# Optimization experiments

Measured on AMD Instinct MI355X. Metric: run time of the kernel, lower is better.

The kernel has to match this reference:

```python
import jax, jax.numpy as jnp
import numpy as np

N, E = 10000, 160000
IN_C, HID, OUT_C, H = 768, 256, 256, 4
EPS = 1e-5


def _gat_layer(x, src, dst, W, a_src, a_dst, b, n_nodes):
    # x: [N, Fin], W: [Fin, H*C], a_src/a_dst: [H, C], b: [C]
    h, c = a_src.shape
    xh = (x @ W).reshape(n_nodes, h, c)                      # [N,H,C]
    s = jnp.einsum('nhc,hc->nh', xh, a_src)                  # [N,H]
    d = jnp.einsum('nhc,hc->nh', xh, a_dst)                  # [N,H]
    e = jax.nn.leaky_relu(s[src] + d[dst], negative_slope=0.2)  # [E,H]
    # segment softmax over incoming edges of each dst node
    emax = jax.ops.segment_max(e, dst, num_segments=n_nodes)
    ex = jnp.exp(e - emax[dst])
    denom = jax.ops.segment_sum(ex, dst, num_segments=n_nodes)
    alpha = ex / denom[dst]                                  # [E,H]
    msg = alpha[:, :, None] * xh[src]                        # [E,H,C]
    out = jax.ops.segment_sum(msg, dst, num_segments=n_nodes)  # [N,H,C]
    return out.mean(axis=1) + b                              # concat=False: head mean


def setup_inputs() -> dict:
    key = jax.random.key(0)
    ks = jax.random.split(key, 12)
    sc1 = 1.0 / np.sqrt(IN_C)
    sc2 = 1.0 / np.sqrt(HID)
    return {
        'x': jax.random.normal(ks[0], (N, IN_C), dtype=jnp.float32),
        'edge_index': jax.random.randint(ks[1], (2, E), 0, N, dtype=jnp.int64),
        'W1': jax.random.normal(ks[2], (IN_C, H * HID), dtype=jnp.float32) * sc1,
        'att_src1': jax.random.normal(ks[3], (H, HID), dtype=jnp.float32) * sc2,
        'att_dst1': jax.random.normal(ks[4], (H, HID), dtype=jnp.float32) * sc2,
        'b1': jnp.zeros((HID,), dtype=jnp.float32),
        'gamma': jnp.ones((HID,), dtype=jnp.float32),
        'beta': jnp.zeros((HID,), dtype=jnp.float32),
        'W2': jax.random.normal(ks[5], (HID, H * OUT_C), dtype=jnp.float32) * sc2,
        'att_src2': jax.random.normal(ks[6], (H, OUT_C), dtype=jnp.float32) * sc2,
        'att_dst2': jax.random.normal(ks[7], (H, OUT_C), dtype=jnp.float32) * sc2,
        'b2': jnp.zeros((OUT_C,), dtype=jnp.float32),
    }


def reference(x, edge_index, W1, att_src1, att_dst1, b1, gamma, beta,
              W2, att_src2, att_dst2, b2):
    n = x.shape[0]
    loops = jnp.arange(n, dtype=edge_index.dtype)  # PyG GATConv adds self-loops
    src = jnp.concatenate([edge_index[0], loops])
    dst = jnp.concatenate([edge_index[1], loops])
    h = _gat_layer(x, src, dst, W1, att_src1, att_dst1, b1, n)   # [N,HID]
    # BatchNorm1d (batch statistics) + ReLU; dropout p=0 is identity
    mu = h.mean(axis=0)
    var = h.var(axis=0)
    h = (h - mu) * jax.lax.rsqrt(var + EPS) * gamma + beta
    h = jax.nn.relu(h)
    return _gat_layer(h, src, dst, W2, att_src2, att_dst2, b2, n)  # [N,OUT_C]
```

## Files before the change

### kernel.cpp

```cpp
#include <hip/hip_runtime.h>
#include <hip/hip_bf16.h>

typedef __bf16 bf16x8 __attribute__((ext_vector_type(8)));
typedef float f32x4 __attribute__((ext_vector_type(4)));
typedef unsigned short ushort8v __attribute__((ext_vector_type(8)));
typedef unsigned short ushort4v __attribute__((ext_vector_type(4)));

#define DEV __device__ __forceinline__

DEV unsigned short f2bf(float f) {
    unsigned u = __builtin_bit_cast(unsigned, f);
    unsigned r = (u + 0x7fffu + ((u >> 16) & 1u)) >> 16;
    return (unsigned short)r;
}

DEV float bf2f(unsigned short b) {
    unsigned u = ((unsigned)b) << 16;
    return __builtin_bit_cast(float, u);
}

DEV float wred_sum(float v) {
    #pragma unroll
    for (int o = 32; o > 0; o >>= 1) v += __shfl_xor(v, o, 64);
    return v;
}

__global__ __launch_bounds__(256) void cvtpad_k(const float* __restrict__ X,
                                                unsigned short* __restrict__ O,
                                                int nrows, int chunks, int ncols, int total) {
    int id = blockIdx.x * 256 + threadIdx.x;
    if (id >= total) return;
    int row = id / chunks;
    int k0 = (id - row * chunks) * 8;
    ushort8v o;
    if (row < nrows) {
        const float* p = X + (size_t)row * ncols + k0;
        float4 a = *(const float4*)p;
        float4 b = *(const float4*)(p + 4);
        o[0] = f2bf(a.x); o[1] = f2bf(a.y); o[2] = f2bf(a.z); o[3] = f2bf(a.w);
        o[4] = f2bf(b.x); o[5] = f2bf(b.y); o[6] = f2bf(b.z); o[7] = f2bf(b.w);
    } else {
        o = (ushort8v)0;
    }
    *(ushort8v*)(O + (size_t)id * 8) = o;
}

__global__ __launch_bounds__(256) void tr_k(const float* __restrict__ W,
                                            unsigned short* __restrict__ WT, int K, int F) {
    __shared__ unsigned short tile[32][33];
    int kb = blockIdx.x * 32, fb = blockIdx.y * 32;
    int tid = threadIdx.x;
    int c = tid & 31;
    #pragma unroll
    for (int i = 0; i < 4; i++) {
        int r = (tid >> 5) + i * 8;
        tile[r][c] = f2bf(W[(size_t)(kb + r) * F + fb + c]);
    }
    __syncthreads();
    #pragma unroll
    for (int i = 0; i < 4; i++) {
        int r = (tid >> 5) + i * 8;
        WT[(size_t)(fb + r) * K + kb + c] = tile[c][r];
    }
}

__global__ __launch_bounds__(256) void hist_k(const int* __restrict__ ei, int* __restrict__ count,
                                              int E, int Et) {
    int id = blockIdx.x * 256 + threadIdx.x;
    if (id >= Et) return;
    int dst = (id < E) ? ei[E + id] : (id - E);
    atomicAdd(&count[dst], 1);
}

__global__ __launch_bounds__(1024) void scan_k(const int* __restrict__ cnt, int* __restrict__ indptr,
                                               int* __restrict__ cursor, int n) {
    __shared__ int wsum[16];
    __shared__ int carry_s;
    int tid = threadIdx.x, wave = tid >> 6, lane = tid & 63;
    if (tid == 0) carry_s = 0;
    __syncthreads();
    for (int base = 0; base < n; base += 1024) {
        int v = (base + tid < n) ? cnt[base + tid] : 0;
        int s = v;
        #pragma unroll
        for (int o = 1; o < 64; o <<= 1) { int t = __shfl_up(s, o, 64); if (lane >= o) s += t; }
        if (lane == 63) wsum[wave] = s;
        __syncthreads();
        if (wave == 0 && lane < 16) {
            int ws = wsum[lane];
            #pragma unroll
            for (int o = 1; o < 16; o <<= 1) { int t = __shfl_up(ws, o, 64); if (lane >= o) ws += t; }
            wsum[lane] = ws;
        }
        __syncthreads();
        int excl = s - v + (wave > 0 ? wsum[wave - 1] : 0) + carry_s;
        if (base + tid < n) { indptr[base + tid] = excl; cursor[base + tid] = excl; }
        __syncthreads();
        if (tid == 0) carry_s += wsum[15];
        __syncthreads();
    }
    if (threadIdx.x == 0) indptr[n] = carry_s;
}

__global__ __launch_bounds__(256) void scatter_k(const int* __restrict__ ei, int* __restrict__ cursor,
                                                 int* __restrict__ srcs, int E, int Et) {
    int id = blockIdx.x * 256 + threadIdx.x;
    if (id >= Et) return;
    int s, d;
    if (id < E) { s = ei[id]; d = ei[E + id]; } else { s = id - E; d = s; }
    int pos = atomicAdd(&cursor[d], 1);
    srcs[pos] = s;
}

__global__ __launch_bounds__(256) void gemm_k(const unsigned short* __restrict__ A,
                                              const unsigned short* __restrict__ B,
                                              unsigned short* __restrict__ C, int K) {
    __shared__ unsigned short lds_a[128 * 64];
    __shared__ unsigned short lds_b[128 * 64];
    int m0 = blockIdx.x * 128, n0 = blockIdx.y * 128;
    int tid = threadIdx.x, wave = tid >> 6, lane = tid & 63;
    int wr = wave >> 1, wc = wave & 1;
    f32x4 acc[4][4] = {};
    int slotbase = wave * 256;
    for (int kt = 0; kt < K; kt += 64) {
        #pragma unroll
        for (int t = 0; t < 4; t++) {
            int slot = slotbase + t * 64 + lane;
            int row = slot >> 3;
            int cp = slot & 7;
            int cc = cp ^ (row & 7);
            const unsigned short* ga = A + (size_t)(m0 + row) * K + kt + cc * 8;
            const unsigned short* gb = B + (size_t)(n0 + row) * K + kt + cc * 8;
            __builtin_amdgcn_global_load_lds((const __attribute__((address_space(1))) void*)ga,
                (__attribute__((address_space(3))) void*)(lds_a + (size_t)(slotbase + t * 64) * 8), 16, 0, 0);
            __builtin_amdgcn_global_load_lds((const __attribute__((address_space(1))) void*)gb,
                (__attribute__((address_space(3))) void*)(lds_b + (size_t)(slotbase + t * 64) * 8), 16, 0, 0);
        }
        __syncthreads();
        #pragma unroll
        for (int kk = 0; kk < 2; kk++) {
            bf16x8 af[4], bg[4];
            #pragma unroll
            for (int m = 0; m < 4; m++) {
                int row = wr * 64 + m * 16 + (lane & 15);
                int c = kk * 4 + (lane >> 4);
                int cp = c ^ (row & 7);
                af[m] = *(const bf16x8*)(lds_a + (row * 8 + cp) * 8);
            }
            #pragma unroll
            for (int nn = 0; nn < 4; nn++) {
                int row = wc * 64 + nn * 16 + (lane & 15);
                int c = kk * 4 + (lane >> 4);
                int cp = c ^ (row & 7);
                bg[nn] = *(const bf16x8*)(lds_b + (row * 8 + cp) * 8);
            }
            #pragma unroll
            for (int m = 0; m < 4; m++)
                #pragma unroll
                for (int nn = 0; nn < 4; nn++)
                    acc[m][nn] = __builtin_amdgcn_mfma_f32_16x16x32_bf16(af[m], bg[nn], acc[m][nn], 0, 0, 0);
        }
        __syncthreads();
    }
    #pragma unroll
    for (int m = 0; m < 4; m++) {
        #pragma unroll
        for (int nn = 0; nn < 4; nn++) {
            int c = n0 + wc * 64 + nn * 16 + (lane & 15);
            #pragma unroll
            for (int j = 0; j < 4; j++) {
                int r = m0 + wr * 64 + m * 16 + (lane >> 4) * 4 + j;
                C[(size_t)r * 1024 + c] = f2bf(acc[m][nn][j]);
            }
        }
    }
}

__global__ __launch_bounds__(256) void sd_k(const unsigned short* __restrict__ xh,
                                            const float* __restrict__ asrc, const float* __restrict__ adst,
                                            float* __restrict__ s, float* __restrict__ d) {
    int n = blockIdx.x;
    int tid = threadIdx.x, h = tid >> 6, lane = tid & 63;
    ushort4v u = *(const ushort4v*)(xh + (size_t)n * 1024 + h * 256 + lane * 4);
    float4 va = *(const float4*)(asrc + h * 256 + lane * 4);
    float4 vd = *(const float4*)(adst + h * 256 + lane * 4);
    float x0 = bf2f(u[0]), x1 = bf2f(u[1]), x2 = bf2f(u[2]), x3 = bf2f(u[3]);
    float ps = x0 * va.x + x1 * va.y + x2 * va.z + x3 * va.w;
    float pd = x0 * vd.x + x1 * vd.y + x2 * vd.z + x3 * vd.w;
    ps = wred_sum(ps);
    pd = wred_sum(pd);
    if (lane == 0) { s[n * 4 + h] = ps; d[n * 4 + h] = pd; }
}

__global__ __launch_bounds__(256) void aggr_k(const unsigned short* __restrict__ xh,
                                              const float* __restrict__ svec, const float* __restrict__ dvec,
                                              const int* __restrict__ indptr, const int* __restrict__ srcs,
                                              const float* __restrict__ bias, float* __restrict__ out) {
    int n = blockIdx.x;
    int tid = threadIdx.x, wave = tid >> 6, lane = tid & 63;
    __shared__ float red[4][4];
    __shared__ float il_s[4], d_s[4];
    __shared__ float alpha_s[256];
    __shared__ int src_s[64];
    __shared__ float ob[2][1024];
    int start = indptr[n];
    int deg = indptr[n + 1] - start;
    if (tid < 4) d_s[tid] = dvec[n * 4 + tid];
    __syncthreads();
    float d0 = d_s[0], d1 = d_s[1], d2 = d_s[2], d3 = d_s[3];
    float l0 = 0, l1 = 0, l2 = 0, l3 = 0;
    for (int i = tid; i < deg; i += 256) {
        int sv = srcs[start + i];
        float4 s4 = *(const float4*)(svec + sv * 4);
        float e0 = s4.x + d0, e1 = s4.y + d1, e2 = s4.z + d2, e3 = s4.w + d3;
        e0 = e0 > 0.f ? e0 : 0.2f * e0; e1 = e1 > 0.f ? e1 : 0.2f * e1;
        e2 = e2 > 0.f ? e2 : 0.2f * e2; e3 = e3 > 0.f ? e3 : 0.2f * e3;
        l0 += __expf(e0); l1 += __expf(e1); l2 += __expf(e2); l3 += __expf(e3);
    }
    l0 = wred_sum(l0); l1 = wred_sum(l1); l2 = wred_sum(l2); l3 = wred_sum(l3);
    if (lane == 0) { red[wave][0] = l0; red[wave][1] = l1; red[wave][2] = l2; red[wave][3] = l3; }
    __syncthreads();
    if (tid == 0) {
        #pragma unroll
        for (int j = 0; j < 4; j++)
            il_s[j] = 0.25f / (red[0][j] + red[1][j] + red[2][j] + red[3][j]);
    }
    __syncthreads();
    int half = tid >> 7;
    int t = tid & 127;
    int head = t >> 5;
    const ushort8v* xb = (const ushort8v*)xh;
    f32x4 acc0 = {0.f, 0.f, 0.f, 0.f}, acc1 = {0.f, 0.f, 0.f, 0.f};
    for (int base = 0; base < deg; base += 64) {
        int cnt = min(64, deg - base);
        if (tid < cnt * 4) {
            int i = tid >> 2, h = tid & 3;
            int sv = srcs[start + base + i];
            if (h == 0) src_s[i] = sv;
            float e = svec[sv * 4 + h] + d_s[h];
            e = e > 0.f ? e : 0.2f * e;
            alpha_s[i * 4 + h] = __expf(e) * il_s[h];
        }
        __syncthreads();
        int i = 0;
        for (; i + 4 <= cnt; i += 4) {
            int ea = i + half * 2, eb = ea + 1;
            int sa = src_s[ea], sb = src_s[eb];
            float aa = alpha_s[ea * 4 + head], ab = alpha_s[eb * 4 + head];
            ushort8v ua = xb[(size_t)sa * 128 + t];
            ushort8v ub = xb[(size_t)sb * 128 + t];
            acc0.x += aa * bf2f(ua[0]) + ab * bf2f(ub[0]);
            acc0.y += aa * bf2f(ua[1]) + ab * bf2f(ub[1]);
            acc0.z += aa * bf2f(ua[2]) + ab * bf2f(ub[2]);
            acc0.w += aa * bf2f(ua[3]) + ab * bf2f(ub[3]);
            acc1.x += aa * bf2f(ua[4]) + ab * bf2f(ub[4]);
            acc1.y += aa * bf2f(ua[5]) + ab * bf2f(ub[5]);
            acc1.z += aa * bf2f(ua[6]) + ab * bf2f(ub[6]);
            acc1.w += aa * bf2f(ua[7]) + ab * bf2f(ub[7]);
        }
        {
            int ea = i + half * 2, eb = ea + 1;
            if (ea < cnt) {
                int sa = src_s[ea];
                float aa = alpha_s[ea * 4 + head];
                ushort8v ua = xb[(size_t)sa * 128 + t];
                acc0.x += aa * bf2f(ua[0]); acc0.y += aa * bf2f(ua[1]);
                acc0.z += aa * bf2f(ua[2]); acc0.w += aa * bf2f(ua[3]);
                acc1.x += aa * bf2f(ua[4]); acc1.y += aa * bf2f(ua[5]);
                acc1.z += aa * bf2f(ua[6]); acc1.w += aa * bf2f(ua[7]);
            }
            if (eb < cnt) {
                int sb = src_s[eb];
                float ab = alpha_s[eb * 4 + head];
                ushort8v ub = xb[(size_t)sb * 128 + t];
                acc0.x += ab * bf2f(ub[0]); acc0.y += ab * bf2f(ub[1]);
                acc0.z += ab * bf2f(ub[2]); acc0.w += ab * bf2f(ub[3]);
                acc1.x += ab * bf2f(ub[4]); acc1.y += ab * bf2f(ub[5]);
                acc1.z += ab * bf2f(ub[6]); acc1.w += ab * bf2f(ub[7]);
            }
        }
        __syncthreads();
    }
    *(f32x4*)(&ob[half][t * 8]) = acc0;
    *(f32x4*)(&ob[half][t * 8 + 4]) = acc1;
    __syncthreads();
    float o = ob[0][tid] + ob[0][256 + tid] + ob[0][512 + tid] + ob[0][768 + tid]
            + ob[1][tid] + ob[1][256 + tid] + ob[1][512 + tid] + ob[1][768 + tid] + bias[tid];
    out[(size_t)n * 256 + tid] = o;
}

__global__ __launch_bounds__(256) void bnstat_k(const float* __restrict__ h, float* __restrict__ bnsum,
                                                float* __restrict__ bnss, int n, int rpb) {
    int c = threadIdx.x;
    int r0 = blockIdx.x * rpb;
    int r1 = min(r0 + rpb, n);
    float s = 0.f, q = 0.f;
    for (int r = r0; r < r1; r++) {
        float v = h[(size_t)r * 256 + c];
        s += v; q += v * v;
    }
    atomicAdd(&bnsum[c], s);
    atomicAdd(&bnss[c], q);
}

__global__ __launch_bounds__(256) void bnapply_k(const float* __restrict__ h, const float* __restrict__ bnsum,
                                                 const float* __restrict__ bnss, const float* __restrict__ gamma,
                                                 const float* __restrict__ beta, unsigned short* __restrict__ o,
                                                 int nrows, float invn) {
    int row = blockIdx.x, c = threadIdx.x;
    unsigned short r;
    if (row < nrows) {
        float mu = bnsum[c] * invn;
        float var = bnss[c] * invn - mu * mu;
        float v = (h[(size_t)row * 256 + c] - mu) * rsqrtf(var + 1e-5f) * gamma[c] + beta[c];
        v = fmaxf(v, 0.f);
        r = f2bf(v);
    } else {
        r = 0;
    }
    o[(size_t)row * 256 + c] = r;
}

extern "C" void kernel_launch(void* const* d_in, const int* in_sizes, int n_in,
                              void* d_out, int out_size, void* d_ws, size_t ws_size,
                              hipStream_t stream) {
    const float* x     = (const float*)d_in[0];
    const int*   ei    = (const int*)d_in[1];
    const float* W1    = (const float*)d_in[2];
    const float* as1   = (const float*)d_in[3];
    const float* ad1   = (const float*)d_in[4];
    const float* b1    = (const float*)d_in[5];
    const float* gamma = (const float*)d_in[6];
    const float* beta  = (const float*)d_in[7];
    const float* W2    = (const float*)d_in[8];
    const float* as2   = (const float*)d_in[9];
    const float* ad2   = (const float*)d_in[10];
    const float* b2    = (const float*)d_in[11];
    float* out = (float*)d_out;

    const int N = in_sizes[0] / 768;
    const int E = in_sizes[1] / 2;
    const int Et = E + N;
    const int Mpad = ((N + 127) / 128) * 128;

    char* w = (char*)d_ws;
    size_t o = 0;
    auto alloc = [&](size_t b) { size_t r = o; o += (b + 255) & ~(size_t)255; return r; };
    unsigned short* xh     = (unsigned short*)(w + alloc((size_t)Mpad * 1024 * 2));
    unsigned short* xbf    = (unsigned short*)(w + alloc((size_t)Mpad * 768 * 2));
    unsigned short* hbf    = (unsigned short*)(w + alloc((size_t)Mpad * 256 * 2));
    unsigned short* w1t    = (unsigned short*)(w + alloc((size_t)1024 * 768 * 2));
    unsigned short* w2t    = (unsigned short*)(w + alloc((size_t)1024 * 256 * 2));
    float*          svec   = (float*)(w + alloc((size_t)N * 4 * 4));
    float*          dvec   = (float*)(w + alloc((size_t)N * 4 * 4));
    float*          hbuf   = (float*)(w + alloc((size_t)N * 256 * 4));
    int*            indptr = (int*)(w + alloc((size_t)(N + 1) * 4));
    int*            cursor = (int*)(w + alloc((size_t)N * 4));
    int*            count  = (int*)(w + alloc((size_t)N * 4));
    float*          bnsum  = (float*)(w + alloc(256 * 4));
    float*          bnss   = (float*)(w + alloc(256 * 4));
    int*            srcs   = (int*)(w + alloc((size_t)Et * 4));

    hipMemsetAsync(count, 0, (size_t)N * 4, stream);
    hipMemsetAsync(bnsum, 0, 2048, stream);

    int cvt_total = Mpad * 96;
    cvtpad_k<<<(cvt_total + 255) / 256, 256, 0, stream>>>(x, xbf, N, 96, 768, cvt_total);
    tr_k<<<dim3(768 / 32, 1024 / 32), 256, 0, stream>>>(W1, w1t, 768, 1024);
    tr_k<<<dim3(256 / 32, 1024 / 32), 256, 0, stream>>>(W2, w2t, 256, 1024);
    hist_k<<<(Et + 255) / 256, 256, 0, stream>>>(ei, count, E, Et);
    scan_k<<<1, 1024, 0, stream>>>(count, indptr, cursor, N);
    scatter_k<<<(Et + 255) / 256, 256, 0, stream>>>(ei, cursor, srcs, E, Et);

    gemm_k<<<dim3(Mpad / 128, 8), 256, 0, stream>>>(xbf, w1t, xh, 768);
    sd_k<<<N, 256, 0, stream>>>(xh, as1, ad1, svec, dvec);
    aggr_k<<<N, 256, 0, stream>>>(xh, svec, dvec, indptr, srcs, b1, hbuf);

    bnstat_k<<<80, 256, 0, stream>>>(hbuf, bnsum, bnss, N, (N + 79) / 80);
    bnapply_k<<<Mpad, 256, 0, stream>>>(hbuf, bnsum, bnss, gamma, beta, hbf, N, 1.0f / (float)N);

    gemm_k<<<dim3(Mpad / 128, 8), 256, 0, stream>>>(hbf, w2t, xh, 256);
    sd_k<<<N, 256, 0, stream>>>(xh, as2, ad2, svec, dvec);
    aggr_k<<<N, 256, 0, stream>>>(xh, svec, dvec, indptr, srcs, b2, out);
}
```

Baseline: 325.2 us.

## Assign one wavefront per node in aggregation and fuse preprocessing kernels

The aggregation kernel now gives each destination node one 64-lane wavefront instead of a 256-thread block. It computes the softmax numerator and denominator in a single pass over the edges, with no shared memory and no block barriers. Each lane holds 16 channels of one head, and the head sum is done with cross-lane shuffles. Separately, the input conversion, the two weight transposes and the degree histogram are merged into one launch to cut launch overhead. The single-pass form drops the max-subtraction (as did the old code) and uses more registers per lane.

```diff
diff --git a/kernel.cpp b/kernel.cpp
--- a/kernel.cpp
+++ b/kernel.cpp
@@ -25,48 +25,54 @@
     return v;
 }
 
-__global__ __launch_bounds__(256) void cvtpad_k(const float* __restrict__ X,
-                                                unsigned short* __restrict__ O,
-                                                int nrows, int chunks, int ncols, int total) {
-    int id = blockIdx.x * 256 + threadIdx.x;
-    if (id >= total) return;
-    int row = id / chunks;
-    int k0 = (id - row * chunks) * 8;
-    ushort8v o;
-    if (row < nrows) {
-        const float* p = X + (size_t)row * ncols + k0;
-        float4 a = *(const float4*)p;
-        float4 b = *(const float4*)(p + 4);
-        o[0] = f2bf(a.x); o[1] = f2bf(a.y); o[2] = f2bf(a.z); o[3] = f2bf(a.w);
-        o[4] = f2bf(b.x); o[5] = f2bf(b.y); o[6] = f2bf(b.z); o[7] = f2bf(b.w);
-    } else {
-        o = (ushort8v)0;
-    }
-    *(ushort8v*)(O + (size_t)id * 8) = o;
-}
-
-__global__ __launch_bounds__(256) void tr_k(const float* __restrict__ W,
-                                            unsigned short* __restrict__ WT, int K, int F) {
+__global__ __launch_bounds__(256) void prep_k(const float* __restrict__ X,
+                                              unsigned short* __restrict__ XO,
+                                              const float* __restrict__ W1, unsigned short* __restrict__ W1T,
+                                              const float* __restrict__ W2, unsigned short* __restrict__ W2T,
+                                              const int* __restrict__ ei, int* __restrict__ count,
+                                              int nrows, int E, int Et,
+                                              int nbA, int nbB, int nbC) {
     __shared__ unsigned short tile[32][33];
-    int kb = blockIdx.x * 32, fb = blockIdx.y * 32;
+    int bid = blockIdx.x;
     int tid = threadIdx.x;
-    int c = tid & 31;
-    #pragma unroll
-    for (int i = 0; i < 4; i++) {
-        int r = (tid >> 5) + i * 8;
-        tile[r][c] = f2bf(W[(size_t)(kb + r) * F + fb + c]);
-    }
-    __syncthreads();
-    #pragma unroll
-    for (int i = 0; i < 4; i++) {
-        int r = (tid >> 5) + i * 8;
-        WT[(size_t)(fb + r) * K + kb + c] = tile[c][r];
-    }
-}
-
-__global__ __launch_bounds__(256) void hist_k(const int* __restrict__ ei, int* __restrict__ count,
-                                              int E, int Et) {
-    int id = blockIdx.x * 256 + threadIdx.x;
+    if (bid < nbA) {
+        int id = bid * 256 + tid;
+        int row = id / 96;
+        int k0 = (id - row * 96) * 8;
+        ushort8v o;
+        if (row < nrows) {
+            const float* p = X + (size_t)row * 768 + k0;
+            float4 a = *(const float4*)p;
+            float4 b = *(const float4*)(p + 4);
+            o[0] = f2bf(a.x); o[1] = f2bf(a.y); o[2] = f2bf(a.z); o[3] = f2bf(a.w);
+            o[4] = f2bf(b.x); o[5] = f2bf(b.y); o[6] = f2bf(b.z); o[7] = f2bf(b.w);
+        } else {
+            o = (ushort8v)0;
+        }
+        *(ushort8v*)(XO + (size_t)id * 8) = o;
+        return;
+    }
+    if (bid < nbA + nbB + nbC) {
+        const float* W; unsigned short* WT; int K, rel;
+        if (bid < nbA + nbB) { W = W1; WT = W1T; K = 768; rel = bid - nbA; }
+        else                 { W = W2; WT = W2T; K = 256; rel = bid - nbA - nbB; }
+        int kdim = K / 32;
+        int kb = (rel % kdim) * 32, fb = (rel / kdim) * 32;
+        int c = tid & 31;
+        #pragma unroll
+        for (int i = 0; i < 4; i++) {
+            int r = (tid >> 5) + i * 8;
+            tile[r][c] = f2bf(W[(size_t)(kb + r) * 1024 + fb + c]);
+        }
+        __syncthreads();
+        #pragma unroll
+        for (int i = 0; i < 4; i++) {
+            int r = (tid >> 5) + i * 8;
+            WT[(size_t)(fb + r) * K + kb + c] = tile[c][r];
+        }
+        return;
+    }
+    int id = (bid - nbA - nbB - nbC) * 256 + tid;
     if (id >= Et) return;
     int dst = (id < E) ? ei[E + id] : (id - E);
     atomicAdd(&count[dst], 1);
@@ -196,97 +202,73 @@
                                               const float* __restrict__ svec, const float* __restrict__ dvec,
                                               const int* __restrict__ indptr, const int* __restrict__ srcs,
                                               const float* __restrict__ bias, float* __restrict__ out) {
-    int n = blockIdx.x;
-    int tid = threadIdx.x, wave = tid >> 6, lane = tid & 63;
-    __shared__ float red[4][4];
-    __shared__ float il_s[4], d_s[4];
-    __shared__ float alpha_s[256];
-    __shared__ int src_s[64];
-    __shared__ float ob[2][1024];
-    int start = indptr[n];
-    int deg = indptr[n + 1] - start;
-    if (tid < 4) d_s[tid] = dvec[n * 4 + tid];
-    __syncthreads();
-    float d0 = d_s[0], d1 = d_s[1], d2 = d_s[2], d3 = d_s[3];
-    float l0 = 0, l1 = 0, l2 = 0, l3 = 0;
-    for (int i = tid; i < deg; i += 256) {
-        int sv = srcs[start + i];
-        float4 s4 = *(const float4*)(svec + sv * 4);
-        float e0 = s4.x + d0, e1 = s4.y + d1, e2 = s4.z + d2, e3 = s4.w + d3;
-        e0 = e0 > 0.f ? e0 : 0.2f * e0; e1 = e1 > 0.f ? e1 : 0.2f * e1;
-        e2 = e2 > 0.f ? e2 : 0.2f * e2; e3 = e3 > 0.f ? e3 : 0.2f * e3;
-        l0 += __expf(e0); l1 += __expf(e1); l2 += __expf(e2); l3 += __expf(e3);
-    }
-    l0 = wred_sum(l0); l1 = wred_sum(l1); l2 = wred_sum(l2); l3 = wred_sum(l3);
-    if (lane == 0) { red[wave][0] = l0; red[wave][1] = l1; red[wave][2] = l2; red[wave][3] = l3; }
-    __syncthreads();
-    if (tid == 0) {
-        #pragma unroll
-        for (int j = 0; j < 4; j++)
-            il_s[j] = 0.25f / (red[0][j] + red[1][j] + red[2][j] + red[3][j]);
-    }
-    __syncthreads();
-    int half = tid >> 7;
-    int t = tid & 127;
-    int head = t >> 5;
+    int n = (blockIdx.x << 2) + (threadIdx.x >> 6);
+    int lane = threadIdx.x & 63;
+    int head = lane >> 4;
+    int start = indptr[n], end = indptr[n + 1];
+    float dh = dvec[n * 4 + head];
     const ushort8v* xb = (const ushort8v*)xh;
-    f32x4 acc0 = {0.f, 0.f, 0.f, 0.f}, acc1 = {0.f, 0.f, 0.f, 0.f};
-    for (int base = 0; base < deg; base += 64) {
-        int cnt = min(64, deg - base);
-        if (tid < cnt * 4) {
-            int i = tid >> 2, h = tid & 3;
-            int sv = srcs[start + base + i];
-            if (h == 0) src_s[i] = sv;
-            float e = svec[sv * 4 + h] + d_s[h];
-            e = e > 0.f ? e : 0.2f * e;
-            alpha_s[i * 4 + h] = __expf(e) * il_s[h];
-        }
-        __syncthreads();
-        int i = 0;
-        for (; i + 4 <= cnt; i += 4) {
-            int ea = i + half * 2, eb = ea + 1;
-            int sa = src_s[ea], sb = src_s[eb];
-            float aa = alpha_s[ea * 4 + head], ab = alpha_s[eb * 4 + head];
-            ushort8v ua = xb[(size_t)sa * 128 + t];
-            ushort8v ub = xb[(size_t)sb * 128 + t];
-            acc0.x += aa * bf2f(ua[0]) + ab * bf2f(ub[0]);
-            acc0.y += aa * bf2f(ua[1]) + ab * bf2f(ub[1]);
-            acc0.z += aa * bf2f(ua[2]) + ab * bf2f(ub[2]);
-            acc0.w += aa * bf2f(ua[3]) + ab * bf2f(ub[3]);
-            acc1.x += aa * bf2f(ua[4]) + ab * bf2f(ub[4]);
-            acc1.y += aa * bf2f(ua[5]) + ab * bf2f(ub[5]);
-            acc1.z += aa * bf2f(ua[6]) + ab * bf2f(ub[6]);
-            acc1.w += aa * bf2f(ua[7]) + ab * bf2f(ub[7]);
-        }
-        {
-            int ea = i + half * 2, eb = ea + 1;
-            if (ea < cnt) {
-                int sa = src_s[ea];
-                float aa = alpha_s[ea * 4 + head];
-                ushort8v ua = xb[(size_t)sa * 128 + t];
-                acc0.x += aa * bf2f(ua[0]); acc0.y += aa * bf2f(ua[1]);
-                acc0.z += aa * bf2f(ua[2]); acc0.w += aa * bf2f(ua[3]);
-                acc1.x += aa * bf2f(ua[4]); acc1.y += aa * bf2f(ua[5]);
-                acc1.z += aa * bf2f(ua[6]); acc1.w += aa * bf2f(ua[7]);
-            }
-            if (eb < cnt) {
-                int sb = src_s[eb];
-                float ab = alpha_s[eb * 4 + head];
-                ushort8v ub = xb[(size_t)sb * 128 + t];
-                acc0.x += ab * bf2f(ub[0]); acc0.y += ab * bf2f(ub[1]);
-                acc0.z += ab * bf2f(ub[2]); acc0.w += ab * bf2f(ub[3]);
-                acc1.x += ab * bf2f(ub[4]); acc1.y += ab * bf2f(ub[5]);
-                acc1.z += ab * bf2f(ub[6]); acc1.w += ab * bf2f(ub[7]);
-            }
-        }
-        __syncthreads();
-    }
-    *(f32x4*)(&ob[half][t * 8]) = acc0;
-    *(f32x4*)(&ob[half][t * 8 + 4]) = acc1;
-    __syncthreads();
-    float o = ob[0][tid] + ob[0][256 + tid] + ob[0][512 + tid] + ob[0][768 + tid]
-            + ob[1][tid] + ob[1][256 + tid] + ob[1][512 + tid] + ob[1][768 + tid] + bias[tid];
-    out[(size_t)n * 256 + tid] = o;
+    size_t loff = (size_t)(lane << 1);
+    float acc[16];
+    #pragma unroll
+    for (int j = 0; j < 16; j++) acc[j] = 0.f;
+    float L = 0.f;
+    int i = start;
+    for (; i + 2 <= end; i += 2) {
+        int s0 = srcs[i], s1 = srcs[i + 1];
+        float e0 = svec[s0 * 4 + head] + dh;
+        float e1 = svec[s1 * 4 + head] + dh;
+        e0 = e0 > 0.f ? e0 : 0.2f * e0;
+        e1 = e1 > 0.f ? e1 : 0.2f * e1;
+        float w0 = __expf(e0), w1 = __expf(e1);
+        L += w0 + w1;
+        ushort8v a0 = xb[(size_t)s0 * 128 + loff];
+        ushort8v a1 = xb[(size_t)s0 * 128 + loff + 1];
+        ushort8v b0 = xb[(size_t)s1 * 128 + loff];
+        ushort8v b1 = xb[(size_t)s1 * 128 + loff + 1];
+        #pragma unroll
+        for (int j = 0; j < 8; j++) {
+            acc[j]     += w0 * bf2f(a0[j]) + w1 * bf2f(b0[j]);
+            acc[8 + j] += w0 * bf2f(a1[j]) + w1 * bf2f(b1[j]);
+        }
+    }
+    if (i < end) {
+        int s0 = srcs[i];
+        float e0 = svec[s0 * 4 + head] + dh;
+        e0 = e0 > 0.f ? e0 : 0.2f * e0;
+        float w0 = __expf(e0);
+        L += w0;
+        ushort8v a0 = xb[(size_t)s0 * 128 + loff];
+        ushort8v a1 = xb[(size_t)s0 * 128 + loff + 1];
+        #pragma unroll
+        for (int j = 0; j < 8; j++) {
+            acc[j]     += w0 * bf2f(a0[j]);
+            acc[8 + j] += w0 * bf2f(a1[j]);
+        }
+    }
+    float inv = 0.25f / L;
+    #pragma unroll
+    for (int j = 0; j < 16; j++) {
+        float r = acc[j] * inv;
+        r += __shfl_xor(r, 16, 64);
+        r += __shfl_xor(r, 32, 64);
+        acc[j] = r;
+    }
+    if (lane < 16) {
+        int c0 = lane << 4;
+        const float4* bp = (const float4*)(bias + c0);
+        float* op = out + (size_t)n * 256 + c0;
+        #pragma unroll
+        for (int q = 0; q < 4; q++) {
+            float4 bv = bp[q];
+            float4 ov;
+            ov.x = acc[q * 4 + 0] + bv.x;
+            ov.y = acc[q * 4 + 1] + bv.y;
+            ov.z = acc[q * 4 + 2] + bv.z;
+            ov.w = acc[q * 4 + 3] + bv.w;
+            *(float4*)(op + q * 4) = ov;
+        }
+    }
 }
 
 __global__ __launch_bounds__(256) void bnstat_k(const float* __restrict__ h, float* __restrict__ bnsum,
@@ -364,22 +346,23 @@
     hipMemsetAsync(count, 0, (size_t)N * 4, stream);
     hipMemsetAsync(bnsum, 0, 2048, stream);
 
-    int cvt_total = Mpad * 96;
-    cvtpad_k<<<(cvt_total + 255) / 256, 256, 0, stream>>>(x, xbf, N, 96, 768, cvt_total);
-    tr_k<<<dim3(768 / 32, 1024 / 32), 256, 0, stream>>>(W1, w1t, 768, 1024);
-    tr_k<<<dim3(256 / 32, 1024 / 32), 256, 0, stream>>>(W2, w2t, 256, 1024);
-    hist_k<<<(Et + 255) / 256, 256, 0, stream>>>(ei, count, E, Et);
+    int nbA = (Mpad * 96) / 256;
+    int nbB = (768 / 32) * (1024 / 32);
+    int nbC = (256 / 32) * (1024 / 32);
+    int nbD = (Et + 255) / 256;
+    prep_k<<<nbA + nbB + nbC + nbD, 256, 0, stream>>>(x, xbf, W1, w1t, W2, w2t, ei, count,
+                                                      N, E, Et, nbA, nbB, nbC);
     scan_k<<<1, 1024, 0, stream>>>(count, indptr, cursor, N);
     scatter_k<<<(Et + 255) / 256, 256, 0, stream>>>(ei, cursor, srcs, E, Et);
 
     gemm_k<<<dim3(Mpad / 128, 8), 256, 0, stream>>>(xbf, w1t, xh, 768);
     sd_k<<<N, 256, 0, stream>>>(xh, as1, ad1, svec, dvec);
-    aggr_k<<<N, 256, 0, stream>>>(xh, svec, dvec, indptr, srcs, b1, hbuf);
+    aggr_k<<<N / 4, 256, 0, stream>>>(xh, svec, dvec, indptr, srcs, b1, hbuf);
 
     bnstat_k<<<80, 256, 0, stream>>>(hbuf, bnsum, bnss, N, (N + 79) / 80);
     bnapply_k<<<Mpad, 256, 0, stream>>>(hbuf, bnsum, bnss, gamma, beta, hbf, N, 1.0f / (float)N);
 
     gemm_k<<<dim3(Mpad / 128, 8), 256, 0, stream>>>(hbf, w2t, xh, 256);
     sd_k<<<N, 256, 0, stream>>>(xh, as2, ad2, svec, dvec);
-    aggr_k<<<N, 256, 0, stream>>>(xh, svec, dvec, indptr, srcs, b2, out);
-}
+    aggr_k<<<N / 4, 256, 0, stream>>>(xh, svec, dvec, indptr, srcs, b2, out);
+}
```

After: 318.5 us. 1.02x faster.
